# Optimization experiments

Measured on AMD Instinct MI355X. Metric: run time of the kernel, lower is better.

## Reference

```python
import jax, jax.numpy as jnp
import numpy as np

DIM = 1024
DIM_HEAD = 64
HEADS = 16
DIM_INNER = DIM_HEAD * HEADS  # 1024


def setup_inputs() -> dict:
    key = jax.random.key(0)
    k1, k2, k3 = jax.random.split(key, 3)
    b, n = 2, 2048
    x = jax.random.normal(k1, (b, n, DIM), dtype=jnp.float32)
    gamma = jnp.ones((DIM,), dtype=jnp.float32)
    # torch Linear weight [out,in] applied as x @ W.T; store pre-transposed [in,out]
    w_qkv = jax.random.normal(k2, (DIM, 3 * DIM_INNER), dtype=jnp.float32) * (DIM ** -0.5)
    w_out = jax.random.normal(k3, (DIM_INNER, DIM), dtype=jnp.float32) * (DIM_INNER ** -0.5)
    return {"x": x, "gamma": gamma, "w_qkv": w_qkv, "w_out": w_out}


def reference(x, gamma, w_qkv, w_out):
    h, d = HEADS, DIM_HEAD
    scale = d ** -0.5
    rms_scale = DIM ** 0.5
    # RMSNorm: F.normalize(x, dim=-1) * sqrt(dim) * gamma  (eps=1e-12 clamp on L2 norm)
    norm = jnp.maximum(jnp.linalg.norm(x, axis=-1, keepdims=True), 1e-12)
    xn = x / norm * rms_scale * gamma
    b, n, _ = x.shape
    qkv = xn @ w_qkv  # [b, n, 3*h*d]
    qkv = qkv.reshape(b, n, 3, h, d)
    q = qkv[:, :, 0].transpose(0, 2, 1, 3) * scale  # [b, h, n, d]
    k = qkv[:, :, 1].transpose(0, 2, 1, 3)
    v = qkv[:, :, 2].transpose(0, 2, 1, 3)
    sim = jnp.einsum('bhid,bhjd->bhij', q, k)  # [b, h, n, n]
    causal_mask = jnp.triu(jnp.ones((n, n), dtype=bool), k=1)
    neg = -jnp.finfo(sim.dtype).max
    sim = jnp.where(causal_mask, neg, sim)
    attn = jax.nn.softmax(sim, axis=-1)
    out = jnp.einsum('bhij,bhjd->bhid', attn, v)  # [b, h, n, d]
    out = out.transpose(0, 2, 1, 3).reshape(b, n, h * d)
    return out @ w_out
```

## Files before the change

kernel.cpp:

```cpp
#include <hip/hip_runtime.h>
#include <hip/hip_bf16.h>

typedef __bf16 bf16x8 __attribute__((ext_vector_type(8)));
typedef short s16x4 __attribute__((ext_vector_type(4)));
typedef float f32x4 __attribute__((ext_vector_type(4)));
typedef unsigned short u16x8 __attribute__((ext_vector_type(8)));

#define MFMA_K32(a, b, c) __builtin_amdgcn_mfma_f32_16x16x32_bf16(a, b, c, 0, 0, 0)

static __device__ __forceinline__ f32x4 mfma_k16(s16x4 a, s16x4 b, f32x4 c) {
#ifdef __HIP_DEVICE_COMPILE__
    return __builtin_amdgcn_mfma_f32_16x16x16bf16_1k(a, b, c, 0, 0, 0);
#else
    return c;
#endif
}

static __device__ __forceinline__ float fast_exp2(float x) {
#ifdef __HIP_DEVICE_COMPILE__
    return __builtin_amdgcn_exp2f(x);
#else
    return x;
#endif
}

#define GLL16(gp, lp)                                              \
    __builtin_amdgcn_global_load_lds(                              \
        (const __attribute__((address_space(1))) void*)(gp),       \
        (__attribute__((address_space(3))) void*)(lp), 16, 0, 0)

static __device__ __forceinline__ unsigned short f2bf(float f) {
    unsigned int u = __float_as_uint(f);
    u += 0x7fffu + ((u >> 16) & 1u);
    return (unsigned short)(u >> 16);
}

static __device__ __forceinline__ unsigned int cvtpk_bf16(float lo, float hi) {
#if defined(__HIP_DEVICE_COMPILE__) && __has_builtin(__builtin_amdgcn_cvt_pk_bf16_f32)
    typedef __bf16 bf16x2 __attribute__((ext_vector_type(2)));
    bf16x2 r = __builtin_amdgcn_cvt_pk_bf16_f32(lo, hi);
    return __builtin_bit_cast(unsigned int, r);
#else
    return (unsigned int)f2bf(lo) | ((unsigned int)f2bf(hi) << 16);
#endif
}

#define LOG2E 1.44269504088896340736f

__global__ __launch_bounds__(256) void prep_k(
    const float* __restrict__ x, const float* __restrict__ gamma,
    const float* __restrict__ w_qkv, const float* __restrict__ w_out,
    unsigned short* __restrict__ xn, unsigned short* __restrict__ wtq,
    unsigned short* __restrict__ wto) {
    __shared__ float sm[32][33];
    int bid = blockIdx.x, tid = threadIdx.x;
    if (bid < 4096) {
        const float* in;
        unsigned short* out;
        int R = 1024, C, bx, by;
        if (bid < 3072) { in = w_qkv; out = wtq; C = 3072; bx = bid % 96; by = bid / 96; }
        else { int b2 = bid - 3072; in = w_out; out = wto; C = 1024; bx = b2 % 32; by = b2 / 32; }
        int c0 = bx * 32, r0 = by * 32;
        int tr = tid >> 5, tc = tid & 31;
#pragma unroll
        for (int i = 0; i < 4; i++)
            sm[tr + i * 8][tc] = in[(size_t)(r0 + tr + i * 8) * C + c0 + tc];
        __syncthreads();
#pragma unroll
        for (int i = 0; i < 4; i++)
            out[(size_t)(c0 + tr + i * 8) * R + r0 + tc] = f2bf(sm[tc][tr + i * 8]);
    } else {
        int row = bid - 4096;
        const float* xr = x + (size_t)row * 1024;
        float4 v = *(const float4*)(xr + tid * 4);
        float ss = v.x * v.x + v.y * v.y + v.z * v.z + v.w * v.w;
#pragma unroll
        for (int off = 1; off < 64; off <<= 1) ss += __shfl_xor(ss, off, 64);
        if ((tid & 63) == 0) sm[0][tid >> 6] = ss;
        __syncthreads();
        float tot = sm[0][0] + sm[0][1] + sm[0][2] + sm[0][3];
        float f = 32.0f / fmaxf(sqrtf(tot), 1e-12f);
        float4 g = *(const float4*)(gamma + tid * 4);
        uint2 o;
        o.x = cvtpk_bf16(v.x * f * g.x, v.y * f * g.y);
        o.y = cvtpk_bf16(v.z * f * g.z, v.w * f * g.w);
        *(uint2*)(xn + (size_t)row * 1024 + tid * 4) = o;
    }
}

template <int MODE, int BM>
__global__ __launch_bounds__(256) void gemm_bt_k(
    const unsigned short* __restrict__ A, const unsigned short* __restrict__ BT,
    float* __restrict__ C, unsigned short* __restrict__ qw,
    unsigned short* __restrict__ kw, unsigned short* __restrict__ vw,
    int M, int N, int K) {
    constexpr int RT = 4;
    constexpr int CT = (BM == 128) ? 4 : 2;
    __shared__ unsigned short As[BM][32];
    __shared__ unsigned short Bs[128][32];
    int tid = threadIdx.x;
    int wave = tid >> 6, lane = tid & 63, quad = lane >> 4, l16 = lane & 15;
    int wrb, wcb;
    if constexpr (BM == 128) { wrb = (wave >> 1) * 64; wcb = (wave & 1) * 64; }
    else { wrb = 0; wcb = wave * 32; }
    int m0 = blockIdx.y * BM, n0 = blockIdx.x * 128;
    int lrow = lane >> 2, lcol = (lane & 3) * 8;
    const unsigned short *Ag0, *Ag1 = nullptr;
    if constexpr (BM == 128) {
        Ag0 = A + (size_t)(m0 + wave * 32 + lrow) * K + lcol;
        Ag1 = A + (size_t)(m0 + wave * 32 + 16 + lrow) * K + lcol;
    } else {
        Ag0 = A + (size_t)(m0 + wave * 16 + lrow) * K + lcol;
    }
    const unsigned short* Bg0 = BT + (size_t)(n0 + wave * 32 + lrow) * K + lcol;
    const unsigned short* Bg1 = BT + (size_t)(n0 + wave * 32 + 16 + lrow) * K + lcol;
    f32x4 acc[RT][CT] = {};
    for (int k0 = 0; k0 < K; k0 += 32) {
        __syncthreads();
        if constexpr (BM == 128) {
            GLL16(Ag0 + k0, &As[wave * 32][0]);
            GLL16(Ag1 + k0, &As[wave * 32 + 16][0]);
        } else {
            GLL16(Ag0 + k0, &As[wave * 16][0]);
        }
        GLL16(Bg0 + k0, &Bs[wave * 32][0]);
        GLL16(Bg1 + k0, &Bs[wave * 32 + 16][0]);
        __syncthreads();
        bf16x8 af[RT], bfr[CT];
#pragma unroll
        for (int t = 0; t < RT; t++)
            af[t] = *(const bf16x8*)&As[wrb + t * 16 + l16][quad * 8];
#pragma unroll
        for (int t = 0; t < CT; t++)
            bfr[t] = *(const bf16x8*)&Bs[wcb + t * 16 + l16][quad * 8];
#pragma unroll
        for (int rt = 0; rt < RT; rt++)
#pragma unroll
            for (int ct = 0; ct < CT; ct++)
                acc[rt][ct] = MFMA_K32(af[rt], bfr[ct], acc[rt][ct]);
    }
#pragma unroll
    for (int rt = 0; rt < RT; rt++) {
        int mb = m0 + wrb + rt * 16 + quad * 4;
        int b = mb >> 11, nn = mb & 2047;
#pragma unroll
        for (int ct = 0; ct < CT; ct++) {
            int col = n0 + wcb + ct * 16 + l16;
            if (MODE == 0) {
#pragma unroll
                for (int r = 0; r < 4; r++)
                    C[(size_t)(mb + r) * N + col] = acc[rt][ct][r];
            } else {
                int sec = col >> 10, ci = col & 1023;
                int hh = ci >> 6, dd = ci & 63;
                int bh = b * 16 + hh;
                if (sec == 0) {
#pragma unroll
                    for (int r = 0; r < 4; r++)
                        qw[((size_t)bh * 2048 + nn + r) * 64 + dd] =
                            f2bf(acc[rt][ct][r] * (0.125f * LOG2E));
                } else if (sec == 1) {
#pragma unroll
                    for (int r = 0; r < 4; r++)
                        kw[((size_t)bh * 2048 + nn + r) * 64 + dd] = f2bf(acc[rt][ct][r]);
                } else {
                    uint2 pk;
                    pk.x = cvtpk_bf16(acc[rt][ct][0], acc[rt][ct][1]);
                    pk.y = cvtpk_bf16(acc[rt][ct][2], acc[rt][ct][3]);
                    *(uint2*)&vw[((size_t)bh * 64 + dd) * 2048 + nn] = pk;
                }
            }
        }
    }
}

__global__ __launch_bounds__(256) void attn_k(
    const unsigned short* __restrict__ q, const unsigned short* __restrict__ k,
    const unsigned short* __restrict__ vt, unsigned short* __restrict__ o) {
    __shared__ unsigned short Ks[2][64][72];
    __shared__ unsigned short Vt[2][64][72];
    int bh = blockIdx.x;
    int qt = 31 - (int)blockIdx.y;
    int tid = threadIdx.x, wave = tid >> 6, lane = tid & 63;
    int quad = lane >> 4, l16 = lane & 15;
    int b = bh >> 4, h = bh & 15;
    const unsigned short* qg = q + (size_t)bh * 2048 * 64;
    const unsigned short* kg = k + (size_t)bh * 2048 * 64;
    const unsigned short* vg = vt + (size_t)bh * 64 * 2048;
    int srow = tid >> 2, scol = (tid & 3) * 16;
    u16x8 pk0, pk1, pv0, pv1;
    int q0w = qt * 64 + wave * 16;
    bf16x8 bq[2];
#pragma unroll
    for (int ks = 0; ks < 2; ks++)
        bq[ks] = *(const bf16x8*)&qg[(size_t)(q0w + l16) * 64 + ks * 32 + quad * 8];
    f32x4 ot[4] = {};
    float mrun = -1e38f, lrun = 0.f;
    int nkt = qt + 1;
    {
        const unsigned short* kp = kg + (size_t)srow * 64 + scol;
        pk0 = *(const u16x8*)kp;
        pk1 = *(const u16x8*)(kp + 8);
        const unsigned short* vp = vg + (size_t)srow * 2048 + scol;
        pv0 = *(const u16x8*)vp;
        pv1 = *(const u16x8*)(vp + 8);
        *(u16x8*)&Ks[0][srow][scol] = pk0;
        *(u16x8*)&Ks[0][srow][scol + 8] = pk1;
        *(u16x8*)&Vt[0][srow][scol] = pv0;
        *(u16x8*)&Vt[0][srow][scol + 8] = pv1;
    }
    __syncthreads();
    for (int kt = 0; kt < nkt; kt++) {
        int cb = kt & 1;
        bool pf = (kt + 1 < nkt);
        if (pf) {
            const unsigned short* kp = kg + (size_t)((kt + 1) * 64 + srow) * 64 + scol;
            pk0 = *(const u16x8*)kp;
            pk1 = *(const u16x8*)(kp + 8);
            const unsigned short* vp = vg + (size_t)srow * 2048 + (kt + 1) * 64 + scol;
            pv0 = *(const u16x8*)vp;
            pv1 = *(const u16x8*)(vp + 8);
        }
        f32x4 sf[4];
#pragma unroll
        for (int ct = 0; ct < 4; ct++) {
            bf16x8 ak0 = *(const bf16x8*)&Ks[cb][ct * 16 + l16][quad * 8];
            bf16x8 ak1 = *(const bf16x8*)&Ks[cb][ct * 16 + l16][32 + quad * 8];
            f32x4 s = {};
            s = MFMA_K32(ak0, bq[0], s);
            s = MFMA_K32(ak1, bq[1], s);
            sf[ct] = s;
        }
        if (kt == qt) {
            int qloc = wave * 16 + l16;
#pragma unroll
            for (int ct = 0; ct < 4; ct++)
#pragma unroll
                for (int r = 0; r < 4; r++)
                    if (ct * 16 + quad * 4 + r > qloc) sf[ct][r] = -1e30f;
        }
        float mx = -1e30f;
#pragma unroll
        for (int ct = 0; ct < 4; ct++)
#pragma unroll
            for (int r = 0; r < 4; r++) mx = fmaxf(mx, sf[ct][r]);
        mx = fmaxf(mx, __shfl_xor(mx, 16, 64));
        mx = fmaxf(mx, __shfl_xor(mx, 32, 64));
        float mnew = fmaxf(mrun, mx);
        float al = fast_exp2(mrun - mnew);
        mrun = mnew;
        float rs = 0.f;
#pragma unroll
        for (int ct = 0; ct < 4; ct++)
#pragma unroll
            for (int r = 0; r < 4; r++) {
                float p = fast_exp2(sf[ct][r] - mnew);
                sf[ct][r] = p;
                rs += p;
            }
        rs += __shfl_xor(rs, 16, 64);
        rs += __shfl_xor(rs, 32, 64);
        lrun = lrun * al + rs;
        s16x4 bpr[4];
#pragma unroll
        for (int ct = 0; ct < 4; ct++) {
            uint2 u;
            u.x = cvtpk_bf16(sf[ct][0], sf[ct][1]);
            u.y = cvtpk_bf16(sf[ct][2], sf[ct][3]);
            bpr[ct] = __builtin_bit_cast(s16x4, u);
        }
#pragma unroll
        for (int dt = 0; dt < 4; dt++) {
#pragma unroll
            for (int r = 0; r < 4; r++) ot[dt][r] *= al;
#pragma unroll
            for (int ct = 0; ct < 4; ct++) {
                s16x4 av = *(const s16x4*)&Vt[cb][dt * 16 + l16][ct * 16 + quad * 4];
                ot[dt] = mfma_k16(av, bpr[ct], ot[dt]);
            }
        }
        if (pf) {
            *(u16x8*)&Ks[1 - cb][srow][scol] = pk0;
            *(u16x8*)&Ks[1 - cb][srow][scol + 8] = pk1;
            *(u16x8*)&Vt[1 - cb][srow][scol] = pv0;
            *(u16x8*)&Vt[1 - cb][srow][scol + 8] = pv1;
        }
        __syncthreads();
    }
    float inv = 1.0f / lrun;
    size_t rowbase = ((size_t)b * 2048 + q0w + l16) * 1024 + h * 64;
#pragma unroll
    for (int dt = 0; dt < 4; dt++) {
        uint2 pk;
        pk.x = cvtpk_bf16(ot[dt][0] * inv, ot[dt][1] * inv);
        pk.y = cvtpk_bf16(ot[dt][2] * inv, ot[dt][3] * inv);
        *(uint2*)&o[rowbase + dt * 16 + quad * 4] = pk;
    }
}

extern "C" void kernel_launch(void* const* d_in, const int* in_sizes, int n_in,
                              void* d_out, int out_size, void* d_ws, size_t ws_size,
                              hipStream_t stream) {
    const float* x = (const float*)d_in[0];
    const float* gamma = (const float*)d_in[1];
    const float* w_qkv = (const float*)d_in[2];
    const float* w_out = (const float*)d_in[3];
    float* out = (float*)d_out;
    char* ws = (char*)d_ws;

    unsigned short* xn = (unsigned short*)(ws);
    unsigned short* wtq = (unsigned short*)(ws + 8388608);
    unsigned short* wto = (unsigned short*)(ws + 14680064);
    unsigned short* qw = (unsigned short*)(ws + 16777216);
    unsigned short* kw = (unsigned short*)(ws + 25165824);
    unsigned short* vw = (unsigned short*)(ws + 33554432);
    unsigned short* ao = xn;

    prep_k<<<8192, 256, 0, stream>>>(x, gamma, w_qkv, w_out, xn, wtq, wto);
    gemm_bt_k<1, 128><<<dim3(24, 32), 256, 0, stream>>>(xn, wtq, nullptr, qw, kw, vw,
                                                        4096, 3072, 1024);
    attn_k<<<dim3(32, 32), 256, 0, stream>>>(qw, kw, vw, ao);
    gemm_bt_k<0, 64><<<dim3(8, 64), 256, 0, stream>>>(ao, wto, out, nullptr, nullptr,
                                                      nullptr, 4096, 1024, 1024);
}
```

Baseline: 191.0 us.

## Split attention KV range across two wave groups with lazy rescale and priority hints

The attention kernel now launches 512 threads per block. Two groups of four waves each process half of the causal key range in 32-key tiles with separate double-buffered LDS, and their partial softmax states are merged through shared memory at the end. It also skips the output rescale unless the running max grows by more than 8 (log2 domain), and raises wave priority around the MFMA sections. The aim is more parallel waves per query tile and less rescale work, at the cost of a combine step and extra LDS traffic.

```diff
diff --git a/kernel.cpp b/kernel.cpp
--- a/kernel.cpp
+++ b/kernel.cpp
@@ -21,6 +21,17 @@
     return __builtin_amdgcn_exp2f(x);
 #else
     return x;
+#endif
+}
+
+static __device__ __forceinline__ void prio_hi() {
+#ifdef __HIP_DEVICE_COMPILE__
+    __builtin_amdgcn_s_setprio(1);
+#endif
+}
+static __device__ __forceinline__ void prio_lo() {
+#ifdef __HIP_DEVICE_COMPILE__
+    __builtin_amdgcn_s_setprio(0);
 #endif
 }
 
@@ -174,127 +185,153 @@
     }
 }
 
-__global__ __launch_bounds__(256) void attn_k(
+__global__ __launch_bounds__(512, 8) void attn_k(
     const unsigned short* __restrict__ q, const unsigned short* __restrict__ k,
     const unsigned short* __restrict__ vt, unsigned short* __restrict__ o) {
-    __shared__ unsigned short Ks[2][64][72];
-    __shared__ unsigned short Vt[2][64][72];
+    __shared__ __align__(16) char smem[38912];
+    typedef unsigned short ush;
+    ush(*Ks)[2][32][72] = (ush(*)[2][32][72])smem;
+    ush(*Vt)[2][64][40] = (ush(*)[2][64][40])(smem + 18432);
+    float(*Osm)[68] = (float(*)[68])smem;
+    float* msm = (float*)(smem + 18432);
+    float* lsm = msm + 64;
+
     int bh = blockIdx.x;
     int qt = 31 - (int)blockIdx.y;
     int tid = threadIdx.x, wave = tid >> 6, lane = tid & 63;
     int quad = lane >> 4, l16 = lane & 15;
+    int g = wave >> 2, wq = wave & 3;
     int b = bh >> 4, h = bh & 15;
-    const unsigned short* qg = q + (size_t)bh * 2048 * 64;
-    const unsigned short* kg = k + (size_t)bh * 2048 * 64;
-    const unsigned short* vg = vt + (size_t)bh * 64 * 2048;
-    int srow = tid >> 2, scol = (tid & 3) * 16;
-    u16x8 pk0, pk1, pv0, pv1;
-    int q0w = qt * 64 + wave * 16;
+    const ush* qg = q + (size_t)bh * 2048 * 64;
+    const ush* kg = k + (size_t)bh * 2048 * 64;
+    const ush* vg = vt + (size_t)bh * 64 * 2048;
+
+    int ti = wq * 64 + lane;
+    int kr = ti >> 3, kc = (ti & 7) * 8;
+    int vr = ti >> 2, vc = (ti & 3) * 8;
+    const ush* Kg = kg + (size_t)kr * 64 + kc;
+    const ush* Vg = vg + (size_t)vr * 2048 + vc;
+
+    int row_l = wq * 16 + l16;
+    int q0w = qt * 64 + wq * 16;
     bf16x8 bq[2];
 #pragma unroll
     for (int ks = 0; ks < 2; ks++)
         bq[ks] = *(const bf16x8*)&qg[(size_t)(q0w + l16) * 64 + ks * 32 + quad * 8];
+
     f32x4 ot[4] = {};
-    float mrun = -1e38f, lrun = 0.f;
-    int nkt = qt + 1;
-    {
-        const unsigned short* kp = kg + (size_t)srow * 64 + scol;
-        pk0 = *(const u16x8*)kp;
-        pk1 = *(const u16x8*)(kp + 8);
-        const unsigned short* vp = vg + (size_t)srow * 2048 + scol;
-        pv0 = *(const u16x8*)vp;
-        pv1 = *(const u16x8*)(vp + 8);
-        *(u16x8*)&Ks[0][srow][scol] = pk0;
-        *(u16x8*)&Ks[0][srow][scol + 8] = pk1;
-        *(u16x8*)&Vt[0][srow][scol] = pv0;
-        *(u16x8*)&Vt[0][srow][scol + 8] = pv1;
-    }
+    float mrun = -1e30f, lrun = 0.f;
+    int nT = qt + 1;
+    int kt0 = g ? (qt + 1) : 0;
+
+    u16x8 pk, pv;
+    pk = *(const u16x8*)(Kg + (size_t)kt0 * 2048);
+    pv = *(const u16x8*)(Vg + kt0 * 32);
+    *(u16x8*)&Ks[g][0][kr][kc] = pk;
+    *(u16x8*)&Vt[g][0][vr][vc] = pv;
     __syncthreads();
-    for (int kt = 0; kt < nkt; kt++) {
-        int cb = kt & 1;
-        bool pf = (kt + 1 < nkt);
+
+    for (int i = 0; i < nT; i++) {
+        int cb = i & 1, kt = kt0 + i;
+        bool pf = (i + 1 < nT);
         if (pf) {
-            const unsigned short* kp = kg + (size_t)((kt + 1) * 64 + srow) * 64 + scol;
-            pk0 = *(const u16x8*)kp;
-            pk1 = *(const u16x8*)(kp + 8);
-            const unsigned short* vp = vg + (size_t)srow * 2048 + (kt + 1) * 64 + scol;
-            pv0 = *(const u16x8*)vp;
-            pv1 = *(const u16x8*)(vp + 8);
-        }
-        f32x4 sf[4];
-#pragma unroll
-        for (int ct = 0; ct < 4; ct++) {
-            bf16x8 ak0 = *(const bf16x8*)&Ks[cb][ct * 16 + l16][quad * 8];
-            bf16x8 ak1 = *(const bf16x8*)&Ks[cb][ct * 16 + l16][32 + quad * 8];
+            pk = *(const u16x8*)(Kg + (size_t)(kt + 1) * 2048);
+            pv = *(const u16x8*)(Vg + (kt + 1) * 32);
+        }
+        f32x4 sf[2];
+        prio_hi();
+#pragma unroll
+        for (int ct = 0; ct < 2; ct++) {
+            bf16x8 ak0 = *(const bf16x8*)&Ks[g][cb][ct * 16 + l16][quad * 8];
+            bf16x8 ak1 = *(const bf16x8*)&Ks[g][cb][ct * 16 + l16][32 + quad * 8];
             f32x4 s = {};
             s = MFMA_K32(ak0, bq[0], s);
             s = MFMA_K32(ak1, bq[1], s);
             sf[ct] = s;
         }
-        if (kt == qt) {
-            int qloc = wave * 16 + l16;
-#pragma unroll
-            for (int ct = 0; ct < 4; ct++)
+        prio_lo();
+        if (kt >= 2 * qt) {
+#pragma unroll
+            for (int ct = 0; ct < 2; ct++)
 #pragma unroll
                 for (int r = 0; r < 4; r++)
-                    if (ct * 16 + quad * 4 + r > qloc) sf[ct][r] = -1e30f;
-        }
-        float mx = -1e30f;
-#pragma unroll
-        for (int ct = 0; ct < 4; ct++)
-#pragma unroll
-            for (int r = 0; r < 4; r++) mx = fmaxf(mx, sf[ct][r]);
+                    if (kt * 32 + ct * 16 + quad * 4 + r > qt * 64 + row_l)
+                        sf[ct][r] = -1e30f;
+        }
+        float m0 = fmaxf(fmaxf(sf[0][0], sf[0][1]), fmaxf(sf[0][2], sf[0][3]));
+        float m1 = fmaxf(fmaxf(sf[1][0], sf[1][1]), fmaxf(sf[1][2], sf[1][3]));
+        float mx = fmaxf(m0, m1);
         mx = fmaxf(mx, __shfl_xor(mx, 16, 64));
         mx = fmaxf(mx, __shfl_xor(mx, 32, 64));
-        float mnew = fmaxf(mrun, mx);
-        float al = fast_exp2(mrun - mnew);
-        mrun = mnew;
+        if (mx > mrun + 8.0f) {
+            float al = fast_exp2(mrun - mx);
+            mrun = mx;
+#pragma unroll
+            for (int dt = 0; dt < 4; dt++)
+#pragma unroll
+                for (int r = 0; r < 4; r++) ot[dt][r] *= al;
+        }
         float rs = 0.f;
 #pragma unroll
-        for (int ct = 0; ct < 4; ct++)
+        for (int ct = 0; ct < 2; ct++)
 #pragma unroll
             for (int r = 0; r < 4; r++) {
-                float p = fast_exp2(sf[ct][r] - mnew);
+                float p = fast_exp2(sf[ct][r] - mrun);
                 sf[ct][r] = p;
                 rs += p;
             }
         rs += __shfl_xor(rs, 16, 64);
         rs += __shfl_xor(rs, 32, 64);
-        lrun = lrun * al + rs;
-        s16x4 bpr[4];
-#pragma unroll
-        for (int ct = 0; ct < 4; ct++) {
+        lrun += rs;
+        s16x4 bpr[2];
+#pragma unroll
+        for (int ct = 0; ct < 2; ct++) {
             uint2 u;
             u.x = cvtpk_bf16(sf[ct][0], sf[ct][1]);
             u.y = cvtpk_bf16(sf[ct][2], sf[ct][3]);
             bpr[ct] = __builtin_bit_cast(s16x4, u);
         }
-#pragma unroll
-        for (int dt = 0; dt < 4; dt++) {
-#pragma unroll
-            for (int r = 0; r < 4; r++) ot[dt][r] *= al;
-#pragma unroll
-            for (int ct = 0; ct < 4; ct++) {
-                s16x4 av = *(const s16x4*)&Vt[cb][dt * 16 + l16][ct * 16 + quad * 4];
+        prio_hi();
+#pragma unroll
+        for (int dt = 0; dt < 4; dt++)
+#pragma unroll
+            for (int ct = 0; ct < 2; ct++) {
+                s16x4 av = *(const s16x4*)&Vt[g][cb][dt * 16 + l16][ct * 16 + quad * 4];
                 ot[dt] = mfma_k16(av, bpr[ct], ot[dt]);
             }
-        }
+        prio_lo();
         if (pf) {
-            *(u16x8*)&Ks[1 - cb][srow][scol] = pk0;
-            *(u16x8*)&Ks[1 - cb][srow][scol + 8] = pk1;
-            *(u16x8*)&Vt[1 - cb][srow][scol] = pv0;
-            *(u16x8*)&Vt[1 - cb][srow][scol + 8] = pv1;
-        }
-        __syncthreads();
-    }
-    float inv = 1.0f / lrun;
-    size_t rowbase = ((size_t)b * 2048 + q0w + l16) * 1024 + h * 64;
-#pragma unroll
-    for (int dt = 0; dt < 4; dt++) {
-        uint2 pk;
-        pk.x = cvtpk_bf16(ot[dt][0] * inv, ot[dt][1] * inv);
-        pk.y = cvtpk_bf16(ot[dt][2] * inv, ot[dt][3] * inv);
-        *(uint2*)&o[rowbase + dt * 16 + quad * 4] = pk;
+            *(u16x8*)&Ks[g][1 - cb][kr][kc] = pk;
+            *(u16x8*)&Vt[g][1 - cb][vr][vc] = pv;
+        }
+        __syncthreads();
+    }
+
+    if (g == 1) {
+        msm[row_l] = mrun;
+        lsm[row_l] = lrun;
+#pragma unroll
+        for (int dt = 0; dt < 4; dt++)
+            *(f32x4*)&Osm[row_l][dt * 16 + quad * 4] = ot[dt];
+    }
+    __syncthreads();
+    if (g == 0) {
+        float m1 = msm[row_l], l1 = lsm[row_l];
+        float mmax = fmaxf(mrun, m1);
+        float a0 = fast_exp2(mrun - mmax), a1 = fast_exp2(m1 - mmax);
+        float inv = 1.0f / (a0 * lrun + a1 * l1);
+        float s0 = a0 * inv, s1 = a1 * inv;
+        size_t rowbase = ((size_t)b * 2048 + qt * 64 + row_l) * 1024 + h * 64;
+#pragma unroll
+        for (int dt = 0; dt < 4; dt++) {
+            f32x4 o1 = *(const f32x4*)&Osm[row_l][dt * 16 + quad * 4];
+            uint2 pkk;
+            pkk.x = cvtpk_bf16(ot[dt][0] * s0 + o1[0] * s1,
+                               ot[dt][1] * s0 + o1[1] * s1);
+            pkk.y = cvtpk_bf16(ot[dt][2] * s0 + o1[2] * s1,
+                               ot[dt][3] * s0 + o1[3] * s1);
+            *(uint2*)&o[rowbase + dt * 16 + quad * 4] = pkk;
+        }
     }
 }
 
@@ -319,7 +356,7 @@
     prep_k<<<8192, 256, 0, stream>>>(x, gamma, w_qkv, w_out, xn, wtq, wto);
     gemm_bt_k<1, 128><<<dim3(24, 32), 256, 0, stream>>>(xn, wtq, nullptr, qw, kw, vw,
                                                         4096, 3072, 1024);
-    attn_k<<<dim3(32, 32), 256, 0, stream>>>(qw, kw, vw, ao);
+    attn_k<<<dim3(32, 32), 512, 0, stream>>>(qw, kw, vw, ao);
     gemm_bt_k<0, 64><<<dim3(8, 64), 256, 0, stream>>>(ao, wto, out, nullptr, nullptr,
                                                       nullptr, 4096, 1024, 1024);
 }
```

Measured after the change: 200.5 us. 1.05x slower.
